# Performance work log

Measured on AMD Instinct MI355X. Metric: run time of the kernel, lower is better.

## Reference

```python
import jax, jax.numpy as jnp
import numpy as np

N, D = 256, 512
DIST_W, ANGLE_W = 1.0, 2.0
EPS_PD = 1e-6    # F.pairwise_distance eps (added to the difference)
EPS_COS = 1e-8   # F.cosine_similarity eps (denominator floor)
CLAMP = 1e-7     # acos clamp margin


def _smooth_l1(x):
    # F.smooth_l1_loss with beta=1.0, elementwise (reduction handled by caller)
    ax = jnp.abs(x)
    return jnp.where(ax < 1.0, 0.5 * ax * ax, ax - 0.5)


def _pairwise_dist(E):
    # Faithful to the looped version: dist[i,j] = ||e_i - e_j + eps|| for i<j,
    # mirrored to the lower triangle, zero diagonal.
    diff = E[:, None, :] - E[None, :, :] + EPS_PD          # [n, n, d]
    d = jnp.sqrt(jnp.sum(diff * diff, axis=-1))            # [n, n]
    upper = jnp.triu(d, k=1)
    return upper + upper.T


def _angles(E):
    # ang[j, i, k] = angle at vertex j between (e_i - e_j) and (e_k - e_j)
    Dv = E[None, :, :] - E[:, None, :]                     # Dv[j, a] = e_a - e_j
    norms = jnp.sqrt(jnp.sum(Dv * Dv, axis=-1))            # [n, n]
    dots = jnp.einsum('jad,jbd->jab', Dv, Dv)              # [n, n, n]
    denom = jnp.maximum(norms[:, :, None] * norms[:, None, :], EPS_COS)
    cos = jnp.clip(dots / denom, -1.0 + CLAMP, 1.0 - CLAMP)
    return jnp.arccos(cos)


def setup_inputs() -> dict:
    key = jax.random.key(0)
    k1, k2 = jax.random.split(key)
    return {
        'student_embeddings': jax.random.normal(k1, (N, D), dtype=jnp.float32),
        'teacher_embeddings': jax.random.normal(k2, (N, D), dtype=jnp.float32),
    }


def reference(student_embeddings, teacher_embeddings):
    # distance-wise loss: smooth_l1 mean over the full n x n matrix
    ds = _pairwise_dist(student_embeddings)
    dt = _pairwise_dist(teacher_embeddings)
    distance_loss = jnp.mean(_smooth_l1(ds - dt))

    # angle-wise loss: mean over triplets i<j<k (vertex at j)
    n = student_embeddings.shape[0]
    ang_s = _angles(student_embeddings)
    ang_t = _angles(teacher_embeddings)
    idx = jnp.arange(n)
    # mask[j, i, k] = (i < j) & (j < k)
    mask = (idx[None, :, None] < idx[:, None, None]) & (idx[:, None, None] < idx[None, None, :])
    count = n * (n - 1) * (n - 2) // 6
    angle_loss = jnp.sum(_smooth_l1(ang_s - ang_t) * mask) / count

    total_loss = DIST_W * distance_loss + ANGLE_W * angle_loss
    return (total_loss, distance_loss, angle_loss)
```

## Files before the change

kernel.cpp:

```cpp
#include <hip/hip_runtime.h>
#include <math.h>

#define N 256
#define D 512
#define SPLIT 4
#define KROW 68

__device__ __forceinline__ float smooth_l1(float x) {
    float ax = fabsf(x);
    return ax < 1.f ? 0.5f * ax * ax : ax - 0.5f;
}

__device__ __forceinline__ float dot4(float4 a, float4 b) {
    return a.x * b.x + a.y * b.y + a.z * b.z + a.w * b.w;
}

__global__ __launch_bounds__(256) void gram_kernel(const float* __restrict__ Es,
                                                   const float* __restrict__ Et,
                                                   float* __restrict__ Gs,
                                                   float* __restrict__ Gt,
                                                   float* __restrict__ acc) {
    const float* E = blockIdx.z ? Et : Es;
    float* G = blockIdx.z ? Gt : Gs;
    const int t = threadIdx.x;

    if (blockIdx.x == 0 && blockIdx.y == 0 && blockIdx.z == 0 && t == 0) {
        acc[0] = 0.f;
        acc[1] = 0.f;
    }

    const int bi = blockIdx.y, bj = blockIdx.x;
    __shared__ __align__(16) float As[32 * KROW];
    __shared__ __align__(16) float Bs[32 * KROW];

    const int tx = t & 15, ty = t >> 4;
    float s00 = 0.f, s01 = 0.f, s10 = 0.f, s11 = 0.f;

    for (int k0 = 0; k0 < D; k0 += 64) {
#pragma unroll
        for (int s = t; s < 512; s += 256) {
            const int r = s >> 4, c = (s & 15) * 4;
            *(float4*)&As[r * KROW + c] = *(const float4*)&E[(bi * 32 + r) * D + k0 + c];
            *(float4*)&Bs[r * KROW + c] = *(const float4*)&E[(bj * 32 + r) * D + k0 + c];
        }
        __syncthreads();
        const float4* A0 = (const float4*)&As[ty * KROW];
        const float4* A1 = (const float4*)&As[(ty + 16) * KROW];
        const float4* B0 = (const float4*)&Bs[tx * KROW];
        const float4* B1 = (const float4*)&Bs[(tx + 16) * KROW];
#pragma unroll
        for (int kk = 0; kk < 16; ++kk) {
            float4 a0 = A0[kk], a1 = A1[kk], b0 = B0[kk], b1 = B1[kk];
            s00 += dot4(a0, b0);
            s01 += dot4(a0, b1);
            s10 += dot4(a1, b0);
            s11 += dot4(a1, b1);
        }
        __syncthreads();
    }

    const int r0 = bi * 32 + ty, r1 = r0 + 16;
    const int c0 = bj * 32 + tx, c1 = c0 + 16;
    G[r0 * N + c0] = s00;
    G[r0 * N + c1] = s01;
    G[r1 * N + c0] = s10;
    G[r1 * N + c1] = s11;
}

__global__ __launch_bounds__(256) void angle_dist_kernel(const float* __restrict__ Gs,
                                                         const float* __restrict__ Gt,
                                                         float* __restrict__ acc) {
    const int j = blockIdx.x + 1;
    const int tid = threadIdx.x;
    __shared__ float2 sv[N], tv[N];
    __shared__ float2 red[256];
    const float Gsjj = Gs[j * N + j];
    const float Gtjj = Gt[j * N + j];

    float distp = 0.f;
    {
        const int a = tid;
        float cja = Gs[a * N + j];
        float cjb = Gt[a * N + j];
        float n2s = Gs[a * N + a] - 2.f * cja + Gsjj;
        float n2t = Gt[a * N + a] - 2.f * cjb + Gtjj;
        float rs = (a == j) ? 0.f : rsqrtf(n2s);
        float rt = (a == j) ? 0.f : rsqrtf(n2t);
        sv[a] = make_float2(cja, rs);
        tv[a] = make_float2(cjb, rt);
        if (blockIdx.y == 0 && a < j)
            distp = smooth_l1(n2s * rs - n2t * rt);
    }
    __syncthreads();

    const int nk = 255 - j;
    const int npairs = j * nk;
    const float inv_nk = 1.0f / (float)nk;
    const float lo = -0.99999994f;
    const float hi = 0.99999994f;

    float anglep = 0.f;
    for (int p = blockIdx.y * 256 + tid; p < npairs; p += 256 * SPLIT) {
        int i = (int)((float)p * inv_nk);
        int rem = p - i * nk;
        if (rem < 0) { --i; rem += nk; }
        else if (rem >= nk) { ++i; rem -= nk; }
        const int k = j + 1 + rem;
        float2 si = sv[i], sk = sv[k];
        float2 ti = tv[i], tk = tv[k];
        float dots = Gs[i * N + k] - si.x - sk.x + Gsjj;
        float dott = Gt[i * N + k] - ti.x - tk.x + Gtjj;
        float coss = fminf(fmaxf(dots * (si.y * sk.y), lo), hi);
        float cost = fminf(fmaxf(dott * (ti.y * tk.y), lo), hi);
        anglep += smooth_l1(acosf(coss) - acosf(cost));
    }

    red[tid] = make_float2(distp, anglep);
    __syncthreads();
    for (int s = 128; s > 0; s >>= 1) {
        if (tid < s) {
            red[tid].x += red[tid + s].x;
            red[tid].y += red[tid + s].y;
        }
        __syncthreads();
    }
    if (tid == 0) {
        atomicAdd(&acc[1], red[0].y);
        if (blockIdx.y == 0) atomicAdd(&acc[0], red[0].x);
    }
}

__global__ void finalize_kernel(const float* __restrict__ acc,
                                float* __restrict__ out) {
    float dl = 2.f * acc[0] / (float)(N * N);
    float al = acc[1] / (float)(N * (N - 1) * (N - 2) / 6);
    out[0] = 1.0f * dl + 2.0f * al;
    out[1] = dl;
    out[2] = al;
}

extern "C" void kernel_launch(void* const* d_in, const int* in_sizes, int n_in,
                              void* d_out, int out_size, void* d_ws, size_t ws_size,
                              hipStream_t stream) {
    const float* Es = (const float*)d_in[0];
    const float* Et = (const float*)d_in[1];
    float* out = (float*)d_out;
    float* ws = (float*)d_ws;

    float* acc = ws;
    float* Gs  = ws + 64;
    float* Gt  = Gs + N * N;

    gram_kernel<<<dim3(8, 8, 2), 256, 0, stream>>>(Es, Et, Gs, Gt, acc);
    angle_dist_kernel<<<dim3(N - 1, SPLIT), 256, 0, stream>>>(Gs, Gt, acc);
    finalize_kernel<<<1, 1, 0, stream>>>(acc, out);
}
```

Baseline: 94.71 us.

## Use bf16 MFMA for Gram, interleave Gram matrices, fast polynomial acos

```diff
diff --git a/kernel.cpp b/kernel.cpp
--- a/kernel.cpp
+++ b/kernel.cpp
@@ -4,90 +4,89 @@
 #define N 256
 #define D 512
 #define SPLIT 4
-#define KROW 68
+
+using f32x4  = __attribute__((ext_vector_type(4))) float;
+using bf16x8 = __attribute__((ext_vector_type(8))) short;
+
+__device__ __forceinline__ short f2bf(float f) {
+    unsigned u = __float_as_uint(f);
+    u += 0x7fffu + ((u >> 16) & 1u);
+    return (short)(u >> 16);
+}
 
 __device__ __forceinline__ float smooth_l1(float x) {
     float ax = fabsf(x);
     return ax < 1.f ? 0.5f * ax * ax : ax - 0.5f;
 }
 
-__device__ __forceinline__ float dot4(float4 a, float4 b) {
-    return a.x * b.x + a.y * b.y + a.z * b.z + a.w * b.w;
+__device__ __forceinline__ float acos_fast(float x) {
+    float ax = fabsf(x);
+    float p = -0.0187293f;
+    p = p * ax + 0.0742610f;
+    p = p * ax - 0.2121144f;
+    p = p * ax + 1.5707288f;
+    float v = sqrtf(1.f - ax) * p;
+    return x < 0.f ? 3.14159265358979f - v : v;
 }
 
-__global__ __launch_bounds__(256) void gram_kernel(const float* __restrict__ Es,
-                                                   const float* __restrict__ Et,
-                                                   float* __restrict__ Gs,
-                                                   float* __restrict__ Gt,
-                                                   float* __restrict__ acc) {
-    const float* E = blockIdx.z ? Et : Es;
-    float* G = blockIdx.z ? Gt : Gs;
-    const int t = threadIdx.x;
-
-    if (blockIdx.x == 0 && blockIdx.y == 0 && blockIdx.z == 0 && t == 0) {
+__global__ __launch_bounds__(64) void gram_kernel(const float* __restrict__ Es,
+                                                  const float* __restrict__ Et,
+                                                  float2* __restrict__ G2,
+                                                  float* __restrict__ acc) {
+    const int lane = threadIdx.x;
+    if (blockIdx.x == 0 && blockIdx.y == 0 && blockIdx.z == 0 && lane == 0) {
         acc[0] = 0.f;
         acc[1] = 0.f;
     }
+    const float* E = blockIdx.z ? Et : Es;
+    const int m = lane & 15, quad = lane >> 4;
+    const int baseA = (blockIdx.y * 16 + m) * D + quad * 8;
+    const int baseB = (blockIdx.x * 16 + m) * D + quad * 8;
 
-    const int bi = blockIdx.y, bj = blockIdx.x;
-    __shared__ __align__(16) float As[32 * KROW];
-    __shared__ __align__(16) float Bs[32 * KROW];
-
-    const int tx = t & 15, ty = t >> 4;
-    float s00 = 0.f, s01 = 0.f, s10 = 0.f, s11 = 0.f;
-
-    for (int k0 = 0; k0 < D; k0 += 64) {
+    f32x4 c = {0.f, 0.f, 0.f, 0.f};
 #pragma unroll
-        for (int s = t; s < 512; s += 256) {
-            const int r = s >> 4, c = (s & 15) * 4;
-            *(float4*)&As[r * KROW + c] = *(const float4*)&E[(bi * 32 + r) * D + k0 + c];
-            *(float4*)&Bs[r * KROW + c] = *(const float4*)&E[(bj * 32 + r) * D + k0 + c];
-        }
-        __syncthreads();
-        const float4* A0 = (const float4*)&As[ty * KROW];
-        const float4* A1 = (const float4*)&As[(ty + 16) * KROW];
-        const float4* B0 = (const float4*)&Bs[tx * KROW];
-        const float4* B1 = (const float4*)&Bs[(tx + 16) * KROW];
-#pragma unroll
-        for (int kk = 0; kk < 16; ++kk) {
-            float4 a0 = A0[kk], a1 = A1[kk], b0 = B0[kk], b1 = B1[kk];
-            s00 += dot4(a0, b0);
-            s01 += dot4(a0, b1);
-            s10 += dot4(a1, b0);
-            s11 += dot4(a1, b1);
-        }
-        __syncthreads();
+    for (int k0 = 0; k0 < D; k0 += 32) {
+        float4 alo = *(const float4*)&E[baseA + k0];
+        float4 ahi = *(const float4*)&E[baseA + k0 + 4];
+        float4 blo = *(const float4*)&E[baseB + k0];
+        float4 bhi = *(const float4*)&E[baseB + k0 + 4];
+        bf16x8 a, b;
+        a[0] = f2bf(alo.x); a[1] = f2bf(alo.y); a[2] = f2bf(alo.z); a[3] = f2bf(alo.w);
+        a[4] = f2bf(ahi.x); a[5] = f2bf(ahi.y); a[6] = f2bf(ahi.z); a[7] = f2bf(ahi.w);
+        b[0] = f2bf(blo.x); b[1] = f2bf(blo.y); b[2] = f2bf(blo.z); b[3] = f2bf(blo.w);
+        b[4] = f2bf(bhi.x); b[5] = f2bf(bhi.y); b[6] = f2bf(bhi.z); b[7] = f2bf(bhi.w);
+        c = __builtin_amdgcn_mfma_f32_16x16x32_bf16(a, b, c, 0, 0, 0);
     }
 
-    const int r0 = bi * 32 + ty, r1 = r0 + 16;
-    const int c0 = bj * 32 + tx, c1 = c0 + 16;
-    G[r0 * N + c0] = s00;
-    G[r0 * N + c1] = s01;
-    G[r1 * N + c0] = s10;
-    G[r1 * N + c1] = s11;
+    const int col = blockIdx.x * 16 + m;
+#pragma unroll
+    for (int r = 0; r < 4; ++r) {
+        const int row = blockIdx.y * 16 + quad * 4 + r;
+        float* slot = (float*)&G2[row * N + col];
+        slot[blockIdx.z] = c[r];
+    }
 }
 
-__global__ __launch_bounds__(256) void angle_dist_kernel(const float* __restrict__ Gs,
-                                                         const float* __restrict__ Gt,
+__global__ __launch_bounds__(256) void angle_dist_kernel(const float2* __restrict__ G2,
                                                          float* __restrict__ acc) {
     const int j = blockIdx.x + 1;
     const int tid = threadIdx.x;
     __shared__ float2 sv[N], tv[N];
     __shared__ float2 red[256];
-    const float Gsjj = Gs[j * N + j];
-    const float Gtjj = Gt[j * N + j];
+    const float2 gjj = G2[j * N + j];
+    const float Gsjj = gjj.x, Gtjj = gjj.y;
 
     float distp = 0.f;
     {
         const int a = tid;
-        float cja = Gs[a * N + j];
-        float cjb = Gt[a * N + j];
-        float n2s = Gs[a * N + a] - 2.f * cja + Gsjj;
-        float n2t = Gt[a * N + a] - 2.f * cjb + Gtjj;
+        float2 gaj = G2[a * N + j];
+        float2 gaa = G2[a * N + a];
+        float n2s = gaa.x - 2.f * gaj.x + Gsjj;
+        float n2t = gaa.y - 2.f * gaj.y + Gtjj;
         float rs = (a == j) ? 0.f : rsqrtf(n2s);
         float rt = (a == j) ? 0.f : rsqrtf(n2t);
-        sv[a] = make_float2(cja, rs);
-        tv[a] = make_float2(cjb, rt);
+        sv[a] = make_float2(gaj.x, rs);
+        tv[a] = make_float2(gaj.y, rt);
         if (blockIdx.y == 0 && a < j)
             distp = smooth_l1(n2s * rs - n2t * rt);
     }
@@ -108,11 +107,12 @@
         const int k = j + 1 + rem;
         float2 si = sv[i], sk = sv[k];
         float2 ti = tv[i], tk = tv[k];
-        float dots = Gs[i * N + k] - si.x - sk.x + Gsjj;
-        float dott = Gt[i * N + k] - ti.x - tk.x + Gtjj;
+        float2 gik = G2[i * N + k];
+        float dots = gik.x - si.x - sk.x + Gsjj;
+        float dott = gik.y - ti.x - tk.x + Gtjj;
         float coss = fminf(fmaxf(dots * (si.y * sk.y), lo), hi);
         float cost = fminf(fmaxf(dott * (ti.y * tk.y), lo), hi);
-        anglep += smooth_l1(acosf(coss) - acosf(cost));
+        anglep += smooth_l1(acos_fast(coss) - acos_fast(cost));
     }
 
     red[tid] = make_float2(distp, anglep);
@@ -148,10 +148,9 @@
     float* ws = (float*)d_ws;
 
     float* acc = ws;
-    float* Gs  = ws + 64;
-    float* Gt  = Gs + N * N;
+    float2* G2 = (float2*)(ws + 64);
 
-    gram_kernel<<<dim3(8, 8, 2), 256, 0, stream>>>(Es, Et, Gs, Gt, acc);
-    angle_dist_kernel<<<dim3(N - 1, SPLIT), 256, 0, stream>>>(Gs, Gt, acc);
+    gram_kernel<<<dim3(16, 16, 2), 64, 0, stream>>>(Es, Et, G2, acc);
+    angle_dist_kernel<<<dim3(N - 1, SPLIT), 256, 0, stream>>>(G2, acc);
     finalize_kernel<<<1, 1, 0, stream>>>(acc, out);
 }
```

After: 86.22 us. -9.0%, faster.
